# Kernel tuning notes

Hardware: AMD Instinct MI355X
Metric: run time of the kernel (lower is better)

The kernel has to match this reference:

```python
import jax, jax.numpy as jnp
import numpy as np

EMBED_DIM = 256
MIN_SCALE = 0.5
BASE = 100.0
NDIM = 3
EPS = 1e-5


def basis_norm(psi, w):
    # w: [B, N] float weights; reduce over token dim (-2)
    norm_sq = jnp.sum(w[..., None] * (psi * psi), axis=-2, keepdims=True)
    return psi / jnp.sqrt(norm_sq + EPS)


def rotary(f, coords, lift):
    # lift: [D//2, 3]; phase: [B, N, D//2]
    phase = coords @ lift.T
    c, s = jnp.cos(phase), jnp.sin(phase)
    f1, f2 = jnp.split(f, 2, axis=-1)
    return jnp.concatenate([f1 * c - f2 * s, f1 * s + f2 * c], axis=-1)


def setup_inputs() -> dict:
    key = jax.random.key(0)
    ks = jax.random.split(key, 12)
    B, N, D = 4, 8192, EMBED_DIM
    phi = jax.random.normal(ks[0], (B, N, D), dtype=jnp.float32)
    coords = jax.random.normal(ks[1], (B, N, NDIM), dtype=jnp.float32)
    weights = jax.random.uniform(ks[2], (B, N), dtype=jnp.float32)
    scale = 1.0 / np.sqrt(D)
    Wq = jax.random.normal(ks[3], (D, D), dtype=jnp.float32) * scale
    bq = jnp.zeros((D,), dtype=jnp.float32)
    Wk = jax.random.normal(ks[4], (D, D), dtype=jnp.float32) * scale
    bk = jax.random.normal(ks[5], (D,), dtype=jnp.float32) * 0.01
    Wv = jax.random.normal(ks[6], (D, D), dtype=jnp.float32) * scale
    bv = jax.random.normal(ks[7], (D,), dtype=jnp.float32) * 0.01
    Wo = jax.random.normal(ks[8], (D, D), dtype=jnp.float32) * scale
    bo = jnp.zeros((D,), dtype=jnp.float32)
    # rotary lift init: k_norms * random unit vecs
    half = D // 2
    scales = BASE ** (-2.0 * np.arange(half) / D)
    k_norms = (2.0 * np.pi / MIN_SCALE) * scales  # [half]
    u = np.asarray(jax.random.normal(ks[9], (half, NDIM)))
    u = u / np.linalg.norm(u, axis=-1, keepdims=True)
    lift = jnp.asarray(k_norms[:, None] * u, dtype=jnp.float32)  # [half, 3]
    return {"phi": phi, "coords": coords, "weights": weights,
            "Wq": Wq, "bq": bq, "Wk": Wk, "bk": bk, "Wv": Wv, "bv": bv,
            "Wo": Wo, "bo": bo, "lift": lift}


def reference(phi, coords, weights, Wq, bq, Wk, bk, Wv, bv, Wo, bo, lift):
    q = phi @ Wq.T + bq
    k = basis_norm(phi @ Wk.T + bk, weights)
    v = basis_norm(phi @ Wv.T + bv, weights)
    q = rotary(q, coords, lift)
    k = rotary(k, coords, lift)
    k = k * weights[..., None]  # float-weights branch
    kv = jnp.einsum('bnd,bne->bde', k, v)   # [B, D, D]
    out = jnp.einsum('bnd,bde->bne', q, kv)  # [B, N, D]
    return out @ Wo.T + bo
```

## Files before the change

kernel.cpp:

```cpp
#include <hip/hip_runtime.h>
#include <hip/hip_bf16.h>
#include <stdint.h>

#define DEV __device__ __forceinline__

typedef short short8 __attribute__((ext_vector_type(8)));
typedef float floatx4 __attribute__((ext_vector_type(4)));
typedef uint32_t uint32x4 __attribute__((ext_vector_type(4)));

constexpr int D = 256;
constexpr int NTOK = 8192;
constexpr int MTOT = 4 * NTOK;

DEV void gl_lds16(const void* g, void* l) {
  __builtin_amdgcn_global_load_lds(
      (const __attribute__((address_space(1))) void*)g,
      (__attribute__((address_space(3))) void*)l, 16, 0, 0);
}

DEV float bflo(uint32_t u) { return __uint_as_float(u << 16); }
DEV float bfhi(uint32_t u) { return __uint_as_float(u & 0xffff0000u); }
DEV uint32_t packbf(float a, float b) {
  uint16_t xa = __builtin_bit_cast(uint16_t, __float2bfloat16(a));
  uint16_t xb = __builtin_bit_cast(uint16_t, __float2bfloat16(b));
  return (uint32_t)xa | ((uint32_t)xb << 16);
}

constexpr int PHI_E = MTOT * D;
constexpr int W_E = D * D;
__global__ __launch_bounds__(256) void convert(
    const float* __restrict__ phi, const float* __restrict__ Wq,
    const float* __restrict__ Wk, const float* __restrict__ Wv,
    uint32_t* __restrict__ dst) {
  const int idx2 = blockIdx.x * 256 + threadIdx.x;
  const int e0 = idx2 * 2;
  float2 v;
  if (e0 < PHI_E) {
    v = ((const float2*)phi)[idx2];
  } else {
    int r = e0 - PHI_E;
    if (r < W_E) v = ((const float2*)Wq)[r >> 1];
    else if (r < 2 * W_E) v = ((const float2*)Wk)[(r - W_E) >> 1];
    else v = ((const float2*)Wv)[(r - 2 * W_E) >> 1];
  }
  dst[idx2] = packbf(v.x, v.y);
}

__global__ __launch_bounds__(256, 2) void gemm_qkv(
    const __hip_bfloat16* __restrict__ phi,
    const __hip_bfloat16* __restrict__ W16,
    const float* __restrict__ bq, const float* __restrict__ bk, const float* __restrict__ bv,
    const float* __restrict__ coords, const float* __restrict__ wts,
    const float* __restrict__ lift,
    __hip_bfloat16* __restrict__ Qb, __hip_bfloat16* __restrict__ Kb,
    __hip_bfloat16* __restrict__ Vb, float* __restrict__ nsk, float* __restrict__ nsv) {
  __shared__ __align__(16) char As[8192];
  __shared__ __align__(16) char Bs[16384];
  const int t = threadIdx.x, lane = t & 63, wid = t >> 6;
  const int wm = (wid & 1) * 64, wn = (wid >> 1) * 64;
  const int l16 = lane & 15, q4 = lane >> 4;
  const int m0 = blockIdx.x * 128;
  const int mat = blockIdx.y;
  const __hip_bfloat16* W = W16 + (size_t)mat * W_E;
  const float* bias = (mat == 0) ? bq : (mat == 1) ? bk : bv;
  __hip_bfloat16* Out = (mat == 0) ? Qb : (mat == 1) ? Kb : Vb;

  floatx4 acc[4][8] = {};

  const int srow = wid * 16 + (lane >> 2);
  const int skoff = (lane & 3) * 8;
  const __hip_bfloat16* gA = phi + (size_t)(m0 + srow) * D + skoff;
  const __hip_bfloat16* gB = W + (size_t)srow * D + skoff;
  char* lA = As + srow * 64 + skoff * 2;
  char* lB = Bs + srow * 64 + skoff * 2;

  for (int kt = 0; kt < 256; kt += 32) {
    gl_lds16(gA + kt, lA);
    gl_lds16(gA + kt + 64 * D, lA + 4096);
    gl_lds16(gB + kt, lB);
    gl_lds16(gB + kt + 64 * D, lB + 4096);
    gl_lds16(gB + kt + 128 * D, lB + 8192);
    gl_lds16(gB + kt + 192 * D, lB + 12288);
    __syncthreads();
    short8 af[4], bf8[8];
#pragma unroll
    for (int i = 0; i < 4; i++)
      af[i] = *(const short8*)(As + (wm + i * 16 + l16) * 64 + q4 * 16);
#pragma unroll
    for (int j = 0; j < 8; j++) {
      const int col = wn + (j & 3) * 16 + (j >> 2) * 128 + l16;
      bf8[j] = *(const short8*)(Bs + col * 64 + q4 * 16);
    }
#pragma unroll
    for (int i = 0; i < 4; i++)
#pragma unroll
      for (int j = 0; j < 8; j++)
        acc[i][j] = __builtin_amdgcn_mfma_f32_16x16x32_bf16(af[i], bf8[j], acc[i][j], 0, 0, 0);
    __syncthreads();
  }

  float bcol[8];
#pragma unroll
  for (int j = 0; j < 8; j++)
    bcol[j] = bias[wn + (j & 3) * 16 + (j >> 2) * 128 + l16];

  if (mat == 0) {
    float lx[4], ly[4], lz[4];
#pragma unroll
    for (int jj = 0; jj < 4; jj++) {
      const int c = wn + jj * 16 + l16;
      lx[jj] = lift[c * 3 + 0]; ly[jj] = lift[c * 3 + 1]; lz[jj] = lift[c * 3 + 2];
    }
#pragma unroll
    for (int i = 0; i < 4; i++) {
#pragma unroll
      for (int r = 0; r < 4; r++) {
        const int row = m0 + wm + i * 16 + q4 * 4 + r;
        const float cx = coords[row * 3 + 0];
        const float cy = coords[row * 3 + 1];
        const float cz = coords[row * 3 + 2];
#pragma unroll
        for (int jj = 0; jj < 4; jj++) {
          const int c = wn + jj * 16 + l16;
          const float p = cx * lx[jj] + cy * ly[jj] + cz * lz[jj];
          float s, cs;
          __sincosf(p, &s, &cs);
          const float f1 = acc[i][jj][r] + bcol[jj];
          const float f2 = acc[i][jj + 4][r] + bcol[jj + 4];
          Out[(size_t)row * D + c]       = __float2bfloat16(f1 * cs - f2 * s);
          Out[(size_t)row * D + c + 128] = __float2bfloat16(f1 * s + f2 * cs);
        }
      }
    }
  } else {
    const int b = m0 >> 13;
    float* ns = (mat == 1) ? nsk : nsv;
    float colsum[8] = {};
#pragma unroll
    for (int i = 0; i < 4; i++) {
#pragma unroll
      for (int r = 0; r < 4; r++) {
        const int row = m0 + wm + i * 16 + q4 * 4 + r;
        const float w = wts[row];
#pragma unroll
        for (int j = 0; j < 8; j++) {
          const int col = wn + (j & 3) * 16 + (j >> 2) * 128 + l16;
          const float psi = acc[i][j][r] + bcol[j];
          Out[(size_t)row * D + col] = __float2bfloat16(psi);
          colsum[j] += w * psi * psi;
        }
      }
    }
#pragma unroll
    for (int j = 0; j < 8; j++) {
      float s = colsum[j];
      s += __shfl_xor(s, 16);
      s += __shfl_xor(s, 32);
      if (q4 == 0) {
        const int col = wn + (j & 3) * 16 + (j >> 2) * 128 + l16;
        atomicAdd(&ns[b * D + col], s);
      }
    }
  }
}

__global__ __launch_bounds__(256, 2) void vproj_pk(
    const __hip_bfloat16* __restrict__ Vb, const float* __restrict__ Wo,
    const float* __restrict__ nsv, __hip_bfloat16* __restrict__ vproj,
    __hip_bfloat16* __restrict__ Kb, const float* __restrict__ coords,
    const float* __restrict__ wts, const float* __restrict__ lift,
    const float* __restrict__ nsk) {
  __shared__ __align__(16) char As[8192];
  __shared__ __align__(16) char Bs[8192];
  __shared__ __align__(16) float isv[256];
  const int bx = blockIdx.x;
  const int t = threadIdx.x;

  if (bx < 512) {
    const int lane = t & 63, wid = t >> 6;
    const int wm = (wid & 1) * 64, wn = (wid >> 1) * 64;
    const int l16 = lane & 15, q4 = lane >> 4;
    const int m0 = (bx >> 1) * 128, n0 = (bx & 1) * 128;
    const int b = m0 >> 13;
    isv[t] = rsqrtf(nsv[b * D + t] + 1e-5f);
    __syncthreads();
    floatx4 acc[4][4] = {};
    const int srow = wid * 16 + (lane >> 2);
    const int skoff = (lane & 3) * 8;
    const __hip_bfloat16* gA = Vb + (size_t)(m0 + srow) * D + skoff;
    const float* gB0 = Wo + (size_t)(n0 + srow) * D + skoff;
    const float* gB1 = Wo + (size_t)(n0 + srow + 64) * D + skoff;
    char* lA = As + srow * 64 + skoff * 2;
    char* lB = Bs + srow * 64 + skoff * 2;
    for (int kt = 0; kt < 256; kt += 32) {
      gl_lds16(gA + kt, lA);
      gl_lds16(gA + kt + 64 * D, lA + 4096);
      const float4 w0 = *(const float4*)(gB0 + kt);
      const float4 w1 = *(const float4*)(gB0 + kt + 4);
      const float4 w2 = *(const float4*)(gB1 + kt);
      const float4 w3 = *(const float4*)(gB1 + kt + 4);
      const float4 i0 = *(const float4*)(&isv[kt + skoff]);
      const float4 i1 = *(const float4*)(&isv[kt + skoff + 4]);
      uint32x4 p0, p1;
      p0[0] = packbf(w0.x * i0.x, w0.y * i0.y);
      p0[1] = packbf(w0.z * i0.z, w0.w * i0.w);
      p0[2] = packbf(w1.x * i1.x, w1.y * i1.y);
      p0[3] = packbf(w1.z * i1.z, w1.w * i1.w);
      p1[0] = packbf(w2.x * i0.x, w2.y * i0.y);
      p1[1] = packbf(w2.z * i0.z, w2.w * i0.w);
      p1[2] = packbf(w3.x * i1.x, w3.y * i1.y);
      p1[3] = packbf(w3.z * i1.z, w3.w * i1.w);
      *(uint32x4*)lB = p0;
      *(uint32x4*)(lB + 4096) = p1;
      __syncthreads();
      short8 af[4], bf8[4];
#pragma unroll
      for (int i = 0; i < 4; i++) {
        af[i]  = *(const short8*)(As + (wm + i * 16 + l16) * 64 + q4 * 16);
        bf8[i] = *(const short8*)(Bs + (wn + i * 16 + l16) * 64 + q4 * 16);
      }
#pragma unroll
      for (int i = 0; i < 4; i++)
#pragma unroll
        for (int j = 0; j < 4; j++)
          acc[i][j] = __builtin_amdgcn_mfma_f32_16x16x32_bf16(af[i], bf8[j], acc[i][j], 0, 0, 0);
      __syncthreads();
    }
#pragma unroll
    for (int j = 0; j < 4; j++) {
      const int colg = n0 + wn + j * 16 + l16;
#pragma unroll
      for (int i = 0; i < 4; i++) {
        const int rowg = m0 + wm + i * 16 + q4 * 4;
#pragma unroll
        for (int r = 0; r < 4; r++)
          vproj[(size_t)(rowg + r) * D + colg] = __float2bfloat16(acc[i][j][r]);
      }
    }
  } else {
    const int j = t & 63, rloc = t >> 6;
    const int pb = bx - 512;
    const int r0 = pb * 256;
    const int b = r0 >> 13;
    const int j0 = 2 * j, j1 = 2 * j + 1;
    const float lx0 = lift[j0 * 3 + 0], ly0 = lift[j0 * 3 + 1], lz0 = lift[j0 * 3 + 2];
    const float lx1 = lift[j1 * 3 + 0], ly1 = lift[j1 * 3 + 1], lz1 = lift[j1 * 3 + 2];
    const int nb = b * D;
    const float ik0 = rsqrtf(nsk[nb + j0] + 1e-5f);
    const float ik1 = rsqrtf(nsk[nb + j1] + 1e-5f);
    const float ik2 = rsqrtf(nsk[nb + 128 + j0] + 1e-5f);
    const float ik3 = rsqrtf(nsk[nb + 128 + j1] + 1e-5f);
    uint32_t* K32 = (uint32_t*)Kb;
    for (int it = 0; it < 64; it++) {
      const size_t row = (size_t)r0 + it * 4 + rloc;
      const float cx = coords[row * 3 + 0];
      const float cy = coords[row * 3 + 1];
      const float cz = coords[row * 3 + 2];
      const float p0 = cx * lx0 + cy * ly0 + cz * lz0;
      const float p1 = cx * lx1 + cy * ly1 + cz * lz1;
      float s0, c0, s1, c1;
      __sincosf(p0, &s0, &c0);
      __sincosf(p1, &s1, &c1);
      const float w = wts[row];
      const size_t base = row * 128;
      const uint32_t klo = K32[base + j], khi = K32[base + 64 + j];
      const float k1a = bflo(klo) * ik0, k1b = bfhi(klo) * ik1;
      const float k2a = bflo(khi) * ik2, k2b = bfhi(khi) * ik3;
      K32[base + j]      = packbf((k1a * c0 - k2a * s0) * w, (k1b * c1 - k2b * s1) * w);
      K32[base + 64 + j] = packbf((k1a * s0 + k2a * c0) * w, (k1b * s1 + k2b * c1) * w);
    }
  }
}

__global__ __launch_bounds__(256, 2) void gemm_tn(
    const __hip_bfloat16* __restrict__ Vp, const __hip_bfloat16* __restrict__ Kwb,
    float* __restrict__ part) {
  __shared__ __align__(16) char sm[2 * 32 * 260];
  char* Asm = sm;
  char* Bsm = sm + 32 * 260;
  const int t = threadIdx.x, lane = t & 63, wid = t >> 6;
  const int wm = (wid & 1) * 64, wn = (wid >> 1) * 64;
  const int l16 = lane & 15, q4 = lane >> 4;
  const int chunk = blockIdx.x;
  const int ed = blockIdx.y, b = blockIdx.z;
  const int e0 = (ed & 1) * 128, d0 = (ed >> 1) * 128;
  const uint32_t* V32 = (const uint32_t*)Vp;
  const uint32_t* K32 = (const uint32_t*)Kwb;
  floatx4 acc[4][4] = {};
  for (int nt = 0; nt < 256; nt += 32) {
    const int nbase = chunk * 256 + nt;
#pragma unroll
    for (int rep = 0; rep < 8; rep++) {
      const int flat = rep * 256 + t;
      const int nn = flat >> 6;
      const int e2 = flat & 63;
      const size_t src = ((size_t)b * NTOK + nbase + nn) * 128;
      *(uint32_t*)(Asm + nn * 260 + e2 * 4) = V32[src + (e0 >> 1) + e2];
      *(uint32_t*)(Bsm + nn * 260 + e2 * 4) = K32[src + (d0 >> 1) + e2];
    }
    __syncthreads();
    short8 af[4], bf8[4];
#pragma unroll
    for (int i = 0; i < 4; i++) {
#pragma unroll
      for (int jj = 0; jj < 8; jj++) {
        af[i][jj]  = *(const short*)(Asm + (q4 * 8 + jj) * 260 + (wm + i * 16 + l16) * 2);
        bf8[i][jj] = *(const short*)(Bsm + (q4 * 8 + jj) * 260 + (wn + i * 16 + l16) * 2);
      }
    }
#pragma unroll
    for (int i = 0; i < 4; i++)
#pragma unroll
      for (int j = 0; j < 4; j++)
        acc[i][j] = __builtin_amdgcn_mfma_f32_16x16x32_bf16(af[i], bf8[j], acc[i][j], 0, 0, 0);
    __syncthreads();
  }
  float* pt = part + (((size_t)(chunk * 4 + b)) << 16);
#pragma unroll
  for (int i = 0; i < 4; i++) {
#pragma unroll
    for (int r = 0; r < 4; r++) {
      const int eg = e0 + wm + i * 16 + q4 * 4 + r;
#pragma unroll
      for (int j = 0; j < 4; j++) {
        const int dg = d0 + wn + j * 16 + l16;
        pt[eg * 256 + dg] = acc[i][j][r];
      }
    }
  }
}

__global__ __launch_bounds__(256) void reduce_kvt(const float* __restrict__ part,
                                                  uint32_t* __restrict__ P) {
  const int flat2 = blockIdx.x * 256 + threadIdx.x;
  const int b = flat2 >> 15;
  const int off2 = flat2 & 32767;
  const float2* p2 = (const float2*)part;
  float sx = 0, sy = 0;
#pragma unroll
  for (int c = 0; c < 32; c++) {
    const float2 v = p2[(((size_t)(c * 4 + b)) << 15) + off2];
    sx += v.x; sy += v.y;
  }
  P[flat2] = packbf(sx, sy);
}

__global__ __launch_bounds__(256, 2) void gemm_out(
    const __hip_bfloat16* __restrict__ A, const __hip_bfloat16* __restrict__ Pm,
    const float* __restrict__ bo, float* __restrict__ Og) {
  __shared__ __align__(16) char As[8192];
  __shared__ __align__(16) char Bs[8192];
  const int t = threadIdx.x, lane = t & 63, wid = t >> 6;
  const int wm = (wid & 1) * 64, wn = (wid >> 1) * 64;
  const int l16 = lane & 15, q4 = lane >> 4;
  const int m0 = blockIdx.x * 128, n0 = blockIdx.y * 128;
  const int b = m0 >> 13;
  const __hip_bfloat16* W = Pm + ((size_t)b << 16);
  floatx4 acc[4][4] = {};
  const int srow = wid * 16 + (lane >> 2);
  const int skoff = (lane & 3) * 8;
  const __hip_bfloat16* gA = A + (size_t)(m0 + srow) * D + skoff;
  const __hip_bfloat16* gB = W + (size_t)(n0 + srow) * D + skoff;
  char* lA = As + srow * 64 + skoff * 2;
  char* lB = Bs + srow * 64 + skoff * 2;
  for (int kt = 0; kt < 256; kt += 32) {
    gl_lds16(gA + kt, lA);
    gl_lds16(gA + kt + 64 * D, lA + 4096);
    gl_lds16(gB + kt, lB);
    gl_lds16(gB + kt + 64 * D, lB + 4096);
    __syncthreads();
    short8 af[4], bf8[4];
#pragma unroll
    for (int i = 0; i < 4; i++) {
      af[i]  = *(const short8*)(As + (wm + i * 16 + l16) * 64 + q4 * 16);
      bf8[i] = *(const short8*)(Bs + (wn + i * 16 + l16) * 64 + q4 * 16);
    }
#pragma unroll
    for (int i = 0; i < 4; i++)
#pragma unroll
      for (int j = 0; j < 4; j++)
        acc[i][j] = __builtin_amdgcn_mfma_f32_16x16x32_bf16(af[i], bf8[j], acc[i][j], 0, 0, 0);
    __syncthreads();
  }
#pragma unroll
  for (int j = 0; j < 4; j++) {
    const int colg = n0 + wn + j * 16 + l16;
    const float bb = bo[colg];
#pragma unroll
    for (int i = 0; i < 4; i++) {
      const int rowg = m0 + wm + i * 16 + q4 * 4;
#pragma unroll
      for (int r = 0; r < 4; r++)
        Og[(size_t)(rowg + r) * D + colg] = acc[i][j][r] + bb;
    }
  }
}

extern "C" void kernel_launch(void* const* d_in, const int* in_sizes, int n_in,
                              void* d_out, int out_size, void* d_ws, size_t ws_size,
                              hipStream_t stream) {
  const float* phi    = (const float*)d_in[0];
  const float* coords = (const float*)d_in[1];
  const float* wts    = (const float*)d_in[2];
  const float* bq     = (const float*)d_in[4];
  const float* bk     = (const float*)d_in[6];
  const float* bv     = (const float*)d_in[8];
  const float* Wo     = (const float*)d_in[9];
  const float* bo     = (const float*)d_in[10];
  const float* lift   = (const float*)d_in[11];

  char* ws = (char*)d_ws;
  __hip_bfloat16* phi16 = (__hip_bfloat16*)ws;
  __hip_bfloat16* W16   = (__hip_bfloat16*)(ws + 16777216);
  const size_t QOFF = 17170432;
  const size_t SZ = (size_t)MTOT * D * 2;
  __hip_bfloat16* Qb = (__hip_bfloat16*)(ws + QOFF);
  __hip_bfloat16* Kb = (__hip_bfloat16*)(ws + QOFF + SZ);
  __hip_bfloat16* Vb = (__hip_bfloat16*)(ws + QOFF + 2 * SZ);
  const size_t NOFF = QOFF + 3 * SZ;
  float* nsk = (float*)(ws + NOFF);
  float* nsv = (float*)(ws + NOFF + 4096);
  float* part = (float*)(ws + NOFF + 8192);
  __hip_bfloat16* P = (__hip_bfloat16*)(ws + NOFF + 8192 + 33554432);
  __hip_bfloat16* vproj = (__hip_bfloat16*)(ws + NOFF + 8192 + 33554432 + 524288);

  hipMemsetAsync(ws + NOFF, 0, 8192, stream);

  convert<<<16768, 256, 0, stream>>>(phi, (const float*)d_in[3], (const float*)d_in[5],
                                     (const float*)d_in[7], (uint32_t*)ws);
  gemm_qkv<<<dim3(256, 3), 256, 0, stream>>>(phi16, W16, bq, bk, bv, coords, wts, lift,
                                             Qb, Kb, Vb, nsk, nsv);
  vproj_pk<<<640, 256, 0, stream>>>(Vb, Wo, nsv, vproj, Kb, coords, wts, lift, nsk);
  gemm_tn<<<dim3(32, 4, 4), 256, 0, stream>>>(vproj, Kb, part);
  reduce_kvt<<<512, 256, 0, stream>>>(part, (uint32_t*)P);
  gemm_out<<<dim3(256, 2), 256, 0, stream>>>(Qb, P, bo, (float*)d_out);
}
```

Before: 196.1 us.

## Transpose gemm_tn LDS tiles for vector reads, store bf16 partials, fold memset

```diff
diff --git a/kernel.cpp b/kernel.cpp
--- a/kernel.cpp
+++ b/kernel.cpp
@@ -31,7 +31,12 @@
 __global__ __launch_bounds__(256) void convert(
     const float* __restrict__ phi, const float* __restrict__ Wq,
     const float* __restrict__ Wk, const float* __restrict__ Wv,
-    uint32_t* __restrict__ dst) {
+    uint32_t* __restrict__ dst, float2* __restrict__ nszero) {
+  if (blockIdx.x == 0) {
+    const float2 z = {0.f, 0.f};
+#pragma unroll
+    for (int k = 0; k < 4; k++) nszero[k * 256 + threadIdx.x] = z;
+  }
   const int idx2 = blockIdx.x * 256 + threadIdx.x;
   const int e0 = idx2 * 2;
   float2 v;
@@ -274,39 +279,44 @@
 
 __global__ __launch_bounds__(256, 2) void gemm_tn(
     const __hip_bfloat16* __restrict__ Vp, const __hip_bfloat16* __restrict__ Kwb,
-    float* __restrict__ part) {
-  __shared__ __align__(16) char sm[2 * 32 * 260];
-  char* Asm = sm;
-  char* Bsm = sm + 32 * 260;
+    __hip_bfloat16* __restrict__ part) {
+  __shared__ __align__(16) char Asm[128 * 80];
+  __shared__ __align__(16) char Bsm[128 * 80];
   const int t = threadIdx.x, lane = t & 63, wid = t >> 6;
   const int wm = (wid & 1) * 64, wn = (wid >> 1) * 64;
   const int l16 = lane & 15, q4 = lane >> 4;
-  const int chunk = blockIdx.x;
-  const int ed = blockIdx.y, b = blockIdx.z;
+  const int chunk = blockIdx.x, ed = blockIdx.y, b = blockIdx.z;
   const int e0 = (ed & 1) * 128, d0 = (ed >> 1) * 128;
   const uint32_t* V32 = (const uint32_t*)Vp;
   const uint32_t* K32 = (const uint32_t*)Kwb;
+  const int s_np = (((t & 3) | ((t >> 6) << 2)) ^ ((t >> 4) & 3));
+  const int s_e2lo = (t >> 2) & 15;
   floatx4 acc[4][4] = {};
   for (int nt = 0; nt < 256; nt += 32) {
     const int nbase = chunk * 256 + nt;
-#pragma unroll
-    for (int rep = 0; rep < 8; rep++) {
-      const int flat = rep * 256 + t;
-      const int nn = flat >> 6;
-      const int e2 = flat & 63;
-      const size_t src = ((size_t)b * NTOK + nbase + nn) * 128;
-      *(uint32_t*)(Asm + nn * 260 + e2 * 4) = V32[src + (e0 >> 1) + e2];
-      *(uint32_t*)(Bsm + nn * 260 + e2 * 4) = K32[src + (d0 >> 1) + e2];
+    const size_t tokbase = ((size_t)b * NTOK + nbase + 2 * s_np) * 128;
+#pragma unroll
+    for (int r = 0; r < 4; r++) {
+      const int e2 = s_e2lo + r * 16;
+      {
+        const uint32_t a0 = V32[tokbase + (e0 >> 1) + e2];
+        const uint32_t a1 = V32[tokbase + 128 + (e0 >> 1) + e2];
+        *(uint32_t*)(Asm + (2 * e2) * 80 + 4 * s_np)     = (a0 & 0xffffu) | (a1 << 16);
+        *(uint32_t*)(Asm + (2 * e2 + 1) * 80 + 4 * s_np) = (a0 >> 16) | (a1 & 0xffff0000u);
+      }
+      {
+        const uint32_t b0 = K32[tokbase + (d0 >> 1) + e2];
+        const uint32_t b1 = K32[tokbase + 128 + (d0 >> 1) + e2];
+        *(uint32_t*)(Bsm + (2 * e2) * 80 + 4 * s_np)     = (b0 & 0xffffu) | (b1 << 16);
+        *(uint32_t*)(Bsm + (2 * e2 + 1) * 80 + 4 * s_np) = (b0 >> 16) | (b1 & 0xffff0000u);
+      }
     }
     __syncthreads();
     short8 af[4], bf8[4];
 #pragma unroll
     for (int i = 0; i < 4; i++) {
-#pragma unroll
-      for (int jj = 0; jj < 8; jj++) {
-        af[i][jj]  = *(const short*)(Asm + (q4 * 8 + jj) * 260 + (wm + i * 16 + l16) * 2);
-        bf8[i][jj] = *(const short*)(Bsm + (q4 * 8 + jj) * 260 + (wn + i * 16 + l16) * 2);
-      }
+      af[i]  = *(const short8*)(Asm + (wm + i * 16 + l16) * 80 + q4 * 16);
+      bf8[i] = *(const short8*)(Bsm + (wn + i * 16 + l16) * 80 + q4 * 16);
     }
 #pragma unroll
     for (int i = 0; i < 4; i++)
@@ -315,7 +325,7 @@
         acc[i][j] = __builtin_amdgcn_mfma_f32_16x16x32_bf16(af[i], bf8[j], acc[i][j], 0, 0, 0);
     __syncthreads();
   }
-  float* pt = part + (((size_t)(chunk * 4 + b)) << 16);
+  __hip_bfloat16* pt = part + (((size_t)(chunk * 4 + b)) << 16);
 #pragma unroll
   for (int i = 0; i < 4; i++) {
 #pragma unroll
@@ -324,23 +334,22 @@
 #pragma unroll
       for (int j = 0; j < 4; j++) {
         const int dg = d0 + wn + j * 16 + l16;
-        pt[eg * 256 + dg] = acc[i][j][r];
-      }
-    }
-  }
-}
-
-__global__ __launch_bounds__(256) void reduce_kvt(const float* __restrict__ part,
+        pt[eg * 256 + dg] = __float2bfloat16(acc[i][j][r]);
+      }
+    }
+  }
+}
+
+__global__ __launch_bounds__(256) void reduce_kvt(const uint32_t* __restrict__ part,
                                                   uint32_t* __restrict__ P) {
   const int flat2 = blockIdx.x * 256 + threadIdx.x;
   const int b = flat2 >> 15;
-  const int off2 = flat2 & 32767;
-  const float2* p2 = (const float2*)part;
+  const int off = flat2 & 32767;
   float sx = 0, sy = 0;
 #pragma unroll
   for (int c = 0; c < 32; c++) {
-    const float2 v = p2[(((size_t)(c * 4 + b)) << 15) + off2];
-    sx += v.x; sy += v.y;
+    const uint32_t u = part[(((size_t)(c * 4 + b)) << 15) + off];
+    sx += bflo(u); sy += bfhi(u);
   }
   P[flat2] = packbf(sx, sy);
 }
@@ -420,18 +429,16 @@
   const size_t NOFF = QOFF + 3 * SZ;
   float* nsk = (float*)(ws + NOFF);
   float* nsv = (float*)(ws + NOFF + 4096);
-  float* part = (float*)(ws + NOFF + 8192);
-  __hip_bfloat16* P = (__hip_bfloat16*)(ws + NOFF + 8192 + 33554432);
-  __hip_bfloat16* vproj = (__hip_bfloat16*)(ws + NOFF + 8192 + 33554432 + 524288);
-
-  hipMemsetAsync(ws + NOFF, 0, 8192, stream);
+  __hip_bfloat16* part = (__hip_bfloat16*)(ws + NOFF + 8192);
+  __hip_bfloat16* P = (__hip_bfloat16*)(ws + NOFF + 8192 + 16777216);
+  __hip_bfloat16* vproj = (__hip_bfloat16*)(ws + NOFF + 8192 + 16777216 + 524288);
 
   convert<<<16768, 256, 0, stream>>>(phi, (const float*)d_in[3], (const float*)d_in[5],
-                                     (const float*)d_in[7], (uint32_t*)ws);
+                                     (const float*)d_in[7], (uint32_t*)ws, (float2*)(ws + NOFF));
   gemm_qkv<<<dim3(256, 3), 256, 0, stream>>>(phi16, W16, bq, bk, bv, coords, wts, lift,
                                              Qb, Kb, Vb, nsk, nsv);
   vproj_pk<<<640, 256, 0, stream>>>(Vb, Wo, nsv, vproj, Kb, coords, wts, lift, nsk);
   gemm_tn<<<dim3(32, 4, 4), 256, 0, stream>>>(vproj, Kb, part);
-  reduce_kvt<<<512, 256, 0, stream>>>(part, (uint32_t*)P);
+  reduce_kvt<<<512, 256, 0, stream>>>((const uint32_t*)part, (uint32_t*)P);
   gemm_out<<<dim3(256, 2), 256, 0, stream>>>(Qb, P, bo, (float*)d_out);
 }
```

Result: faster. 191.0 us (-2.6%).
